# Kernel optimization log

Measured on AMD Instinct MI355X. Metric: run time of the kernel, lower is better.

## Reference

```python
import jax, jax.numpy as jnp
import numpy as np

N = 50000      # num_nodes
E = 12500      # num hyperedges
NNZ = 400000   # incidence pairs
OBS = 64
LAT = 64
STEPS = 20     # (t1 - t0) / dt = 1.0 / 0.05
DT = 0.05
SQRT_DT = DT ** 0.5
SIGMA_INIT = 0.1


def setup_inputs() -> dict:
    key = jax.random.key(0)
    ks = jax.random.split(key, 12)
    w = lambda k, o, i: jax.random.normal(k, (o, i), dtype=jnp.float32) * (1.0 / np.sqrt(i))
    return {
        "x": jax.random.normal(ks[0], (N, OBS), dtype=jnp.float32),
        "enc_w1": w(ks[1], LAT, OBS),
        "enc_b1": jnp.zeros((LAT,), jnp.float32),
        "enc_w2": w(ks[2], LAT, LAT),
        "enc_b2": jnp.zeros((LAT,), jnp.float32),
        "conv_w": w(ks[3], LAT, LAT),
        "conv_b": jnp.zeros((LAT,), jnp.float32),
        "sigma": SIGMA_INIT * jnp.ones((LAT,), jnp.float32),
        "dec_w1": w(ks[4], LAT, LAT),
        "dec_b1": jnp.zeros((LAT,), jnp.float32),
        "dec_w2": w(ks[5], OBS, LAT),
        "dec_b2": jnp.zeros((OBS,), jnp.float32),
        "node_idx": jax.random.randint(ks[6], (NNZ,), 0, N),
        "edge_idx": jax.random.randint(ks[7], (NNZ,), 0, E),
        "seed": 0,
    }


def _mlp(x, w1, b1, w2, b2):
    # eqx.nn.MLP depth=1: linear -> relu -> linear, applied per node (vmapped == matmul)
    return jax.nn.relu(x @ w1.T + b1) @ w2.T + b2


def reference(x, enc_w1, enc_b1, enc_w2, enc_b2, conv_w, conv_b, sigma,
              dec_w1, dec_b1, dec_w2, dec_b2, node_idx, edge_idx, seed):
    # incidence degree normalization (HGNN-style), computed once
    ones = jnp.ones((NNZ,), jnp.float32)
    edge_deg_inv = 1.0 / jnp.maximum(jax.ops.segment_sum(ones, edge_idx, num_segments=E), 1.0)
    node_deg_inv = 1.0 / jnp.maximum(jax.ops.segment_sum(ones, node_idx, num_segments=N), 1.0)

    def conv(y):
        m = y @ conv_w.T                                                    # [N, LAT]
        e = jax.ops.segment_sum(m[node_idx], edge_idx, num_segments=E)     # node -> hyperedge
        e = e * edge_deg_inv[:, None]
        out = jax.ops.segment_sum(e[edge_idx], node_idx, num_segments=N)   # hyperedge -> node
        return out * node_deg_inv[:, None] + conv_b

    def step(y, k):
        dw = jax.random.normal(k, (N, LAT), dtype=y.dtype)
        drift = jnp.tanh(conv(y))                       # activation(conv) drift
        y = y + drift * DT + sigma * SQRT_DT * dw       # Euler-Maruyama, diagonal noise
        return y, None

    z0 = _mlp(x, enc_w1, enc_b1, enc_w2, enc_b2)        # encode (n, obs) -> (n, lat)
    keys = jax.random.split(jax.random.key(seed), STEPS)
    z1, _ = jax.lax.scan(step, z0, keys)
    return _mlp(z1, dec_w1, dec_b1, dec_w2, dec_b2)     # decode at t1
```

## Files before the change

kernel.cpp:

```cpp
#include <hip/hip_runtime.h>
#include <stdint.h>

#define N_NODES 50000
#define N_EDGES 12500
#define NNZV    400000
#define STEPS   20
#define DT_F    0.05f
#define SQRTDT_F 0.22360679774997896f

__device__ __forceinline__ float rdlf(float v, int l) {
  return __uint_as_float(__builtin_amdgcn_readlane(__float_as_uint(v), (unsigned)l));
}
__device__ __forceinline__ int rfl(int v) {
  return (int)__builtin_amdgcn_readfirstlane((unsigned)v);
}

__device__ __forceinline__ void tf2x32(uint32_t k0, uint32_t k1,
                                       uint32_t x0, uint32_t x1,
                                       uint32_t& o0, uint32_t& o1) {
  uint32_t k2 = k0 ^ k1 ^ 0x1BD11BDAu;
#define TFR(r) { x0 += x1; x1 = (x1 << (r)) | (x1 >> (32 - (r))); x1 ^= x0; }
  x0 += k0; x1 += k1;
  TFR(13) TFR(15) TFR(26) TFR(6)   x0 += k1; x1 += k2 + 1u;
  TFR(17) TFR(29) TFR(16) TFR(24)  x0 += k2; x1 += k0 + 2u;
  TFR(13) TFR(15) TFR(26) TFR(6)   x0 += k0; x1 += k1 + 3u;
  TFR(17) TFR(29) TFR(16) TFR(24)  x0 += k1; x1 += k2 + 4u;
  TFR(13) TFR(15) TFR(26) TFR(6)   x0 += k2; x1 += k0 + 5u;
#undef TFR
  o0 = x0; o1 = x1;
}

__device__ __forceinline__ float erfinv_fast(float x) {
  float w = -__logf((1.0f - x) * (1.0f + x));
  float p;
  if (w < 5.0f) {
    w = w - 2.5f;
    p =              2.81022636e-08f;
    p = fmaf(p, w,   3.43273939e-07f);
    p = fmaf(p, w,  -3.5233877e-06f);
    p = fmaf(p, w,  -4.39150654e-06f);
    p = fmaf(p, w,   0.00021858087f);
    p = fmaf(p, w,  -0.00125372503f);
    p = fmaf(p, w,  -0.00417768164f);
    p = fmaf(p, w,   0.246640727f);
    p = fmaf(p, w,   1.50140941f);
  } else {
    w = sqrtf(w) - 3.0f;
    p =             -0.000200214257f;
    p = fmaf(p, w,   0.000100950558f);
    p = fmaf(p, w,   0.00134934322f);
    p = fmaf(p, w,  -0.00367342844f);
    p = fmaf(p, w,   0.00573950773f);
    p = fmaf(p, w,  -0.0076224613f);
    p = fmaf(p, w,   0.00943887047f);
    p = fmaf(p, w,   1.00167406f);
    p = fmaf(p, w,   2.83297682f);
  }
  return p * x;
}

__device__ __forceinline__ float bits_to_normal(uint32_t b) {
  float f = __uint_as_float((b >> 9) | 0x3f800000u) - 1.0f;
  const float lo = -0.99999994f;
  float u = fmaf(f, 2.0f, lo);
  u = fmaxf(u, lo);
  return 1.41421356237f * erfinv_fast(u);
}

__device__ __forceinline__ float fast_tanhf(float x) {
  float t = __expf(2.0f * x);
  return 1.0f - 2.0f / (t + 1.0f);
}

__global__ void k_keys(const int* __restrict__ seed, unsigned* __restrict__ keys) {
  int j = threadIdx.x;
  if (j < STEPS) {
    unsigned s = (unsigned)seed[0];
    unsigned o0, o1;
    tf2x32(0u, s, 0u, (unsigned)j, o0, o1);
    keys[2 * j] = o0; keys[2 * j + 1] = o1;
  }
}

__global__ void k_zero(int* __restrict__ p, int n) {
  int i = blockIdx.x * 256 + threadIdx.x;
  if (i < n) p[i] = 0;
}

__global__ void k_hist(const int* __restrict__ nidx, const int* __restrict__ eidx,
                       int* __restrict__ ecnt, int* __restrict__ ncnt) {
  int i = blockIdx.x * 256 + threadIdx.x;
  if (i < NNZV) {
    atomicAdd(&ecnt[eidx[i]], 1);
    atomicAdd(&ncnt[nidx[i]], 1);
  }
}

__global__ __launch_bounds__(256) void k_reduce(const int* __restrict__ cnt, int len,
                                                int* __restrict__ bsum) {
  __shared__ int sh[256];
  int b = blockIdx.x, tid = threadIdx.x;
  int base = b * 1024 + tid * 4;
  int s = 0;
#pragma unroll
  for (int j = 0; j < 4; ++j) {
    int i = base + j;
    if (i < len) s += cnt[i];
  }
  sh[tid] = s;
  __syncthreads();
  for (int off = 128; off > 0; off >>= 1) {
    if (tid < off) sh[tid] += sh[tid + off];
    __syncthreads();
  }
  if (tid == 0) bsum[b] = sh[0];
}

__global__ __launch_bounds__(256) void k_scanb(int* __restrict__ bsum, int nb) {
  __shared__ int sh[256];
  int tid = threadIdx.x;
  int v = (tid < nb) ? bsum[tid] : 0;
  sh[tid] = v;
  __syncthreads();
  for (int off = 1; off < 256; off <<= 1) {
    int t = (tid >= off) ? sh[tid - off] : 0;
    __syncthreads();
    sh[tid] += t;
    __syncthreads();
  }
  if (tid < nb) bsum[tid] = sh[tid] - v;
}

__global__ __launch_bounds__(256) void k_scatter(const int* __restrict__ cnt,
                                                 const int* __restrict__ bsum, int len,
                                                 int* __restrict__ start,
                                                 int* __restrict__ fill,
                                                 float* __restrict__ dinv) {
  __shared__ int sh[256];
  int b = blockIdx.x, tid = threadIdx.x;
  int base = b * 1024 + tid * 4;
  int c[4], lex[4];
  int s = 0;
#pragma unroll
  for (int j = 0; j < 4; ++j) {
    int i = base + j;
    c[j] = (i < len) ? cnt[i] : 0;
    lex[j] = s;
    s += c[j];
  }
  sh[tid] = s;
  __syncthreads();
  for (int off = 1; off < 256; off <<= 1) {
    int t = (tid >= off) ? sh[tid - off] : 0;
    __syncthreads();
    sh[tid] += t;
    __syncthreads();
  }
  int off0 = bsum[b] + sh[tid] - s;
#pragma unroll
  for (int j = 0; j < 4; ++j) {
    int i = base + j;
    if (i < len) {
      start[i] = off0 + lex[j];
      fill[i] = 0;
      dinv[i] = 1.0f / (float)(c[j] > 1 ? c[j] : 1);
    }
  }
}

__global__ void k_fill(const int* __restrict__ nidx, const int* __restrict__ eidx,
                       const int* __restrict__ estart, const int* __restrict__ nstart,
                       int* __restrict__ efill, int* __restrict__ nfill,
                       int* __restrict__ emem, int* __restrict__ nmem) {
  int i = blockIdx.x * 256 + threadIdx.x;
  if (i < NNZV) {
    int e = eidx[i], n = nidx[i];
    int pe = atomicAdd(&efill[e], 1);
    emem[estart[e] + pe] = n;
    int pn = atomicAdd(&nfill[n], 1);
    nmem[nstart[n] + pn] = e;
  }
}

__device__ __forceinline__ void stage_swz(const float* __restrict__ w,
                                          float* __restrict__ lds, int tid) {
  for (int idx = tid; idx < 4096; idx += 256) {
    int j = idx >> 6, k = idx & 63;
    lds[k * 64 + (j ^ k)] = w[idx];
  }
}

__device__ __forceinline__ void seg_gather_dual(const float* __restrict__ rows,
                                                const int* __restrict__ mem,
                                                int st0, int d0, int st1, int d1,
                                                int lane, float& out0, float& out1) {
  float a0 = 0.f, a1 = 0.f, b0 = 0.f, b1 = 0.f;
  int i0 = 0, i1 = 0;
  while (i0 + 8 <= d0 && i1 + 8 <= d1) {
    int A0 = mem[st0 + i0],     A1 = mem[st0 + i0 + 1];
    int A2 = mem[st0 + i0 + 2], A3 = mem[st0 + i0 + 3];
    int A4 = mem[st0 + i0 + 4], A5 = mem[st0 + i0 + 5];
    int A6 = mem[st0 + i0 + 6], A7 = mem[st0 + i0 + 7];
    int B0 = mem[st1 + i1],     B1 = mem[st1 + i1 + 1];
    int B2 = mem[st1 + i1 + 2], B3 = mem[st1 + i1 + 3];
    int B4 = mem[st1 + i1 + 4], B5 = mem[st1 + i1 + 5];
    int B6 = mem[st1 + i1 + 6], B7 = mem[st1 + i1 + 7];
    float x0 = rows[(size_t)A0 * 64 + lane], x1 = rows[(size_t)A1 * 64 + lane];
    float x2 = rows[(size_t)A2 * 64 + lane], x3 = rows[(size_t)A3 * 64 + lane];
    float x4 = rows[(size_t)A4 * 64 + lane], x5 = rows[(size_t)A5 * 64 + lane];
    float x6 = rows[(size_t)A6 * 64 + lane], x7 = rows[(size_t)A7 * 64 + lane];
    float z0 = rows[(size_t)B0 * 64 + lane], z1 = rows[(size_t)B1 * 64 + lane];
    float z2 = rows[(size_t)B2 * 64 + lane], z3 = rows[(size_t)B3 * 64 + lane];
    float z4 = rows[(size_t)B4 * 64 + lane], z5 = rows[(size_t)B5 * 64 + lane];
    float z6 = rows[(size_t)B6 * 64 + lane], z7 = rows[(size_t)B7 * 64 + lane];
    a0 += (x0 + x1) + (x2 + x3);
    a1 += (x4 + x5) + (x6 + x7);
    b0 += (z0 + z1) + (z2 + z3);
    b1 += (z4 + z5) + (z6 + z7);
    i0 += 8; i1 += 8;
  }
  for (; i0 + 8 <= d0; i0 += 8) {
    int A0 = mem[st0 + i0],     A1 = mem[st0 + i0 + 1];
    int A2 = mem[st0 + i0 + 2], A3 = mem[st0 + i0 + 3];
    int A4 = mem[st0 + i0 + 4], A5 = mem[st0 + i0 + 5];
    int A6 = mem[st0 + i0 + 6], A7 = mem[st0 + i0 + 7];
    float x0 = rows[(size_t)A0 * 64 + lane], x1 = rows[(size_t)A1 * 64 + lane];
    float x2 = rows[(size_t)A2 * 64 + lane], x3 = rows[(size_t)A3 * 64 + lane];
    float x4 = rows[(size_t)A4 * 64 + lane], x5 = rows[(size_t)A5 * 64 + lane];
    float x6 = rows[(size_t)A6 * 64 + lane], x7 = rows[(size_t)A7 * 64 + lane];
    a0 += (x0 + x1) + (x2 + x3);
    a1 += (x4 + x5) + (x6 + x7);
  }
  for (; i0 < d0; ++i0) a0 += rows[(size_t)mem[st0 + i0] * 64 + lane];
  for (; i1 + 8 <= d1; i1 += 8) {
    int B0 = mem[st1 + i1],     B1 = mem[st1 + i1 + 1];
    int B2 = mem[st1 + i1 + 2], B3 = mem[st1 + i1 + 3];
    int B4 = mem[st1 + i1 + 4], B5 = mem[st1 + i1 + 5];
    int B6 = mem[st1 + i1 + 6], B7 = mem[st1 + i1 + 7];
    float z0 = rows[(size_t)B0 * 64 + lane], z1 = rows[(size_t)B1 * 64 + lane];
    float z2 = rows[(size_t)B2 * 64 + lane], z3 = rows[(size_t)B3 * 64 + lane];
    float z4 = rows[(size_t)B4 * 64 + lane], z5 = rows[(size_t)B5 * 64 + lane];
    float z6 = rows[(size_t)B6 * 64 + lane], z7 = rows[(size_t)B7 * 64 + lane];
    b0 += (z0 + z1) + (z2 + z3);
    b1 += (z4 + z5) + (z6 + z7);
  }
  for (; i1 < d1; ++i1) b0 += rows[(size_t)mem[st1 + i1] * 64 + lane];
  out0 = a0 + a1;
  out1 = b0 + b1;
}

__global__ __launch_bounds__(256) void k_encoder(
    const float* __restrict__ x, const float* __restrict__ w1,
    const float* __restrict__ b1, const float* __restrict__ w2,
    const float* __restrict__ b2, float* __restrict__ y) {
  __shared__ float lw1[4096], lw2[4096];
  int tid = threadIdx.x;
  stage_swz(w1, lw1, tid);
  stage_swz(w2, lw2, tid);
  __syncthreads();
  int lane = tid & 63, wave = tid >> 6;
  float w1r[64], w2r[64];
#pragma unroll
  for (int k = 0; k < 64; ++k) {
    w1r[k] = lw1[k * 64 + (lane ^ k)];
    w2r[k] = lw2[k * 64 + (lane ^ k)];
  }
  float b1v = b1[lane], b2v = b2[lane];
  int gw = blockIdx.x * 4 + wave, nw = gridDim.x * 4;
  for (int n = gw; n < N_NODES; n += nw) {
    float xv = x[(size_t)n * 64 + lane];
    float a0 = 0.f, a1 = 0.f, a2 = 0.f, a3 = 0.f;
#pragma unroll
    for (int k = 0; k < 64; k += 4) {
      a0 = fmaf(rdlf(xv, k),     w1r[k],     a0);
      a1 = fmaf(rdlf(xv, k + 1), w1r[k + 1], a1);
      a2 = fmaf(rdlf(xv, k + 2), w1r[k + 2], a2);
      a3 = fmaf(rdlf(xv, k + 3), w1r[k + 3], a3);
    }
    float h = fmaxf((a0 + a1) + (a2 + a3) + b1v, 0.f);
    a0 = a1 = a2 = a3 = 0.f;
#pragma unroll
    for (int k = 0; k < 64; k += 4) {
      a0 = fmaf(rdlf(h, k),     w2r[k],     a0);
      a1 = fmaf(rdlf(h, k + 1), w2r[k + 1], a1);
      a2 = fmaf(rdlf(h, k + 2), w2r[k + 2], a2);
      a3 = fmaf(rdlf(h, k + 3), w2r[k + 3], a3);
    }
    y[(size_t)n * 64 + lane] = (a0 + a1) + (a2 + a3) + b2v;
  }
}

__global__ __launch_bounds__(256) void k_edge(
    const float* __restrict__ y, float* __restrict__ e,
    const int* __restrict__ estart, const int* __restrict__ ecnt,
    const int* __restrict__ emem, const float* __restrict__ edinv,
    const float* __restrict__ cw) {
  __shared__ float lcw[4096];
  int tid = threadIdx.x;
  stage_swz(cw, lcw, tid);
  __syncthreads();
  int lane = tid & 63, wave = tid >> 6;
  const int NE2 = N_EDGES / 2;
  int gw = blockIdx.x * 4 + wave, nw = gridDim.x * 4;
  for (int p = gw; p < NE2; p += nw) {
    int p0 = rfl(p);
    int e0 = p0, e1 = p0 + NE2;
    int st0 = estart[e0], d0 = ecnt[e0];
    int st1 = estart[e1], d1 = ecnt[e1];
    float div0 = edinv[e0], div1 = edinv[e1];
    float s0, s1;
    seg_gather_dual(y, emem, st0, d0, st1, d1, lane, s0, s1);
    float a00 = 0.f, a01 = 0.f, a10 = 0.f, a11 = 0.f;
#pragma unroll
    for (int k = 0; k < 64; k += 2) {
      float w0 = lcw[k * 64 + (lane ^ k)];
      float w1 = lcw[(k + 1) * 64 + (lane ^ (k + 1))];
      a00 = fmaf(rdlf(s0, k),     w0, a00);
      a10 = fmaf(rdlf(s1, k),     w0, a10);
      a01 = fmaf(rdlf(s0, k + 1), w1, a01);
      a11 = fmaf(rdlf(s1, k + 1), w1, a11);
    }
    e[(size_t)e0 * 64 + lane] = (a00 + a01) * div0;
    e[(size_t)e1 * 64 + lane] = (a10 + a11) * div1;
  }
}

__global__ __launch_bounds__(256) void k_node(
    const float* __restrict__ e, float* __restrict__ y,
    const int* __restrict__ nstart, const int* __restrict__ ncnt,
    const int* __restrict__ nmem, const float* __restrict__ ndinv,
    const float* __restrict__ cb, const float* __restrict__ sigma,
    const unsigned* __restrict__ keys, int s) {
  int tid = threadIdx.x;
  int lane = tid & 63, wave = tid >> 6;
  float cbv = cb[lane];
  float sgv = sigma[lane] * SQRTDT_F;
  unsigned ka = keys[2 * s], kb = keys[2 * s + 1];
  const int NP = N_NODES / 2;
  int gw = blockIdx.x * 4 + wave, nw = gridDim.x * 4;
  for (int p = gw; p < NP; p += nw) {
    int p0 = rfl(p);
    int n0 = p0, n1 = p0 + NP;
    int st0 = nstart[n0], d0 = ncnt[n0];
    int st1 = nstart[n1], d1 = ncnt[n1];
    float di0 = ndinv[n0], di1 = ndinv[n1];
    float y0 = y[(size_t)n0 * 64 + lane];
    float y1 = y[(size_t)n1 * 64 + lane];
    float s0, s1;
    seg_gather_dual(e, nmem, st0, d0, st1, d1, lane, s0, s1);
    uint32_t r0, r1, r2, r3;
    tf2x32(ka, kb, 0u, (unsigned)(n0 * 64 + lane), r0, r1);
    tf2x32(ka, kb, 0u, (unsigned)(n1 * 64 + lane), r2, r3);
    float dw0 = bits_to_normal(r0 ^ r1);
    float dw1 = bits_to_normal(r2 ^ r3);
    y0 = fmaf(fast_tanhf(fmaf(s0, di0, cbv)), DT_F, fmaf(sgv, dw0, y0));
    y1 = fmaf(fast_tanhf(fmaf(s1, di1, cbv)), DT_F, fmaf(sgv, dw1, y1));
    y[(size_t)n0 * 64 + lane] = y0;
    y[(size_t)n1 * 64 + lane] = y1;
  }
}

__global__ __launch_bounds__(256) void k_decoder(
    const float* __restrict__ y, const float* __restrict__ w1,
    const float* __restrict__ b1, const float* __restrict__ w2,
    const float* __restrict__ b2, float* __restrict__ out) {
  __shared__ float lw1[4096], lw2[4096];
  int tid = threadIdx.x;
  stage_swz(w1, lw1, tid);
  stage_swz(w2, lw2, tid);
  __syncthreads();
  int lane = tid & 63, wave = tid >> 6;
  float w1r[64], w2r[64];
#pragma unroll
  for (int k = 0; k < 64; ++k) {
    w1r[k] = lw1[k * 64 + (lane ^ k)];
    w2r[k] = lw2[k * 64 + (lane ^ k)];
  }
  float b1v = b1[lane], b2v = b2[lane];
  int gw = blockIdx.x * 4 + wave, nw = gridDim.x * 4;
  for (int n = gw; n < N_NODES; n += nw) {
    float xv = y[(size_t)n * 64 + lane];
    float a0 = 0.f, a1 = 0.f, a2 = 0.f, a3 = 0.f;
#pragma unroll
    for (int k = 0; k < 64; k += 4) {
      a0 = fmaf(rdlf(xv, k),     w1r[k],     a0);
      a1 = fmaf(rdlf(xv, k + 1), w1r[k + 1], a1);
      a2 = fmaf(rdlf(xv, k + 2), w1r[k + 2], a2);
      a3 = fmaf(rdlf(xv, k + 3), w1r[k + 3], a3);
    }
    float h = fmaxf((a0 + a1) + (a2 + a3) + b1v, 0.f);
    a0 = a1 = a2 = a3 = 0.f;
#pragma unroll
    for (int k = 0; k < 64; k += 4) {
      a0 = fmaf(rdlf(h, k),     w2r[k],     a0);
      a1 = fmaf(rdlf(h, k + 1), w2r[k + 1], a1);
      a2 = fmaf(rdlf(h, k + 2), w2r[k + 2], a2);
      a3 = fmaf(rdlf(h, k + 3), w2r[k + 3], a3);
    }
    out[(size_t)n * 64 + lane] = (a0 + a1) + (a2 + a3) + b2v;
  }
}

extern "C" void kernel_launch(void* const* d_in, const int* in_sizes, int n_in,
                              void* d_out, int out_size, void* d_ws, size_t ws_size,
                              hipStream_t stream) {
  (void)in_sizes; (void)n_in; (void)out_size; (void)ws_size;
  const float* x      = (const float*)d_in[0];
  const float* enc_w1 = (const float*)d_in[1];
  const float* enc_b1 = (const float*)d_in[2];
  const float* enc_w2 = (const float*)d_in[3];
  const float* enc_b2 = (const float*)d_in[4];
  const float* conv_w = (const float*)d_in[5];
  const float* conv_b = (const float*)d_in[6];
  const float* sigma  = (const float*)d_in[7];
  const float* dec_w1 = (const float*)d_in[8];
  const float* dec_b1 = (const float*)d_in[9];
  const float* dec_w2 = (const float*)d_in[10];
  const float* dec_b2 = (const float*)d_in[11];
  const int* node_idx = (const int*)d_in[12];
  const int* edge_idx = (const int*)d_in[13];
  const int* seed     = (const int*)d_in[14];

  char* wsb = (char*)d_ws;
  size_t off = 0;
  auto alloc = [&](size_t bytes) -> void* {
    void* p = wsb + off;
    off = (off + bytes + 255) & ~(size_t)255;
    return p;
  };
  float* y        = (float*)alloc((size_t)N_NODES * 64 * 4);
  float* e        = (float*)alloc((size_t)N_EDGES * 64 * 4);
  int* edge_cnt   = (int*)alloc((size_t)N_EDGES * 4);
  int* node_cnt   = (int*)alloc((size_t)N_NODES * 4);
  int* edge_start = (int*)alloc((size_t)N_EDGES * 4);
  int* node_start = (int*)alloc((size_t)N_NODES * 4);
  int* edge_fill  = (int*)alloc((size_t)N_EDGES * 4);
  int* node_fill  = (int*)alloc((size_t)N_NODES * 4);
  int* edge_mem   = (int*)alloc((size_t)NNZV * 4);
  int* node_mem   = (int*)alloc((size_t)NNZV * 4);
  float* edinv    = (float*)alloc((size_t)N_EDGES * 4);
  float* ndinv    = (float*)alloc((size_t)N_NODES * 4);
  unsigned* keys  = (unsigned*)alloc(2 * STEPS * 4);
  int* ebsum      = (int*)alloc(256 * 4);
  int* nbsum      = (int*)alloc(256 * 4);

  const int EB = (N_EDGES + 1023) / 1024;
  const int NB = (N_NODES + 1023) / 1024;

  dim3 b256(256);
  hipLaunchKernelGGL(k_keys, dim3(1), dim3(64), 0, stream, seed, keys);
  hipLaunchKernelGGL(k_zero, dim3((N_EDGES + 255) / 256), b256, 0, stream, edge_cnt, N_EDGES);
  hipLaunchKernelGGL(k_zero, dim3((N_NODES + 255) / 256), b256, 0, stream, node_cnt, N_NODES);
  hipLaunchKernelGGL(k_hist, dim3((NNZV + 255) / 256), b256, 0, stream,
                     node_idx, edge_idx, edge_cnt, node_cnt);
  hipLaunchKernelGGL(k_reduce, dim3(EB), b256, 0, stream, edge_cnt, N_EDGES, ebsum);
  hipLaunchKernelGGL(k_reduce, dim3(NB), b256, 0, stream, node_cnt, N_NODES, nbsum);
  hipLaunchKernelGGL(k_scanb, dim3(1), b256, 0, stream, ebsum, EB);
  hipLaunchKernelGGL(k_scanb, dim3(1), b256, 0, stream, nbsum, NB);
  hipLaunchKernelGGL(k_scatter, dim3(EB), b256, 0, stream,
                     edge_cnt, ebsum, N_EDGES, edge_start, edge_fill, edinv);
  hipLaunchKernelGGL(k_scatter, dim3(NB), b256, 0, stream,
                     node_cnt, nbsum, N_NODES, node_start, node_fill, ndinv);
  hipLaunchKernelGGL(k_fill, dim3((NNZV + 255) / 256), b256, 0, stream,
                     node_idx, edge_idx, edge_start, node_start,
                     edge_fill, node_fill, edge_mem, node_mem);
  hipLaunchKernelGGL(k_encoder, dim3(1024), b256, 0, stream,
                     x, enc_w1, enc_b1, enc_w2, enc_b2, y);
  for (int s = 0; s < STEPS; ++s) {
    hipLaunchKernelGGL(k_edge, dim3(1563), b256, 0, stream,
                       y, e, edge_start, edge_cnt, edge_mem, edinv, conv_w);
    hipLaunchKernelGGL(k_node, dim3(2048), b256, 0, stream,
                       e, y, node_start, node_cnt, node_mem, ndinv,
                       conv_b, sigma, keys, s);
  }
  hipLaunchKernelGGL(k_decoder, dim3(1024), b256, 0, stream,
                     y, dec_w1, dec_b1, dec_w2, dec_b2, (float*)d_out);
}
```

Baseline: 1.097 ms.

## Fuse SDE time-step loop into one persistent cooperative kernel with grid sync

Replaces the 40 separate edge/node kernel launches with one cooperative persistent kernel that loops over all steps, using grid-wide barriers between the edge-gather and node-update phases. Conv weights are staged into LDS once instead of every step. This removes per-launch overhead and the kernel-boundary drain between phases. In exchange, the grid is limited by occupancy, which may lower parallelism per phase, and adds grid.sync costs. The old launches remain as a fallback if the cooperative launch fails.

Measured after the change: 4.321 ms. +293.8%, slower.

```diff
diff --git a/kernel.cpp b/kernel.cpp
--- a/kernel.cpp
+++ b/kernel.cpp
@@ -1,5 +1,8 @@
 #include <hip/hip_runtime.h>
+#include <hip/hip_cooperative_groups.h>
 #include <stdint.h>
+
+namespace cg = cooperative_groups;
 
 #define N_NODES 50000
 #define N_EDGES 12500
@@ -290,18 +293,12 @@
   }
 }
 
-__global__ __launch_bounds__(256) void k_edge(
+__device__ __forceinline__ void edge_body(
     const float* __restrict__ y, float* __restrict__ e,
     const int* __restrict__ estart, const int* __restrict__ ecnt,
     const int* __restrict__ emem, const float* __restrict__ edinv,
-    const float* __restrict__ cw) {
-  __shared__ float lcw[4096];
-  int tid = threadIdx.x;
-  stage_swz(cw, lcw, tid);
-  __syncthreads();
-  int lane = tid & 63, wave = tid >> 6;
+    const float* __restrict__ lcw, int lane, int gw, int nw) {
   const int NE2 = N_EDGES / 2;
-  int gw = blockIdx.x * 4 + wave, nw = gridDim.x * 4;
   for (int p = gw; p < NE2; p += nw) {
     int p0 = rfl(p);
     int e0 = p0, e1 = p0 + NE2;
@@ -325,19 +322,12 @@
   }
 }
 
-__global__ __launch_bounds__(256) void k_node(
+__device__ __forceinline__ void node_body(
     const float* __restrict__ e, float* __restrict__ y,
     const int* __restrict__ nstart, const int* __restrict__ ncnt,
     const int* __restrict__ nmem, const float* __restrict__ ndinv,
-    const float* __restrict__ cb, const float* __restrict__ sigma,
-    const unsigned* __restrict__ keys, int s) {
-  int tid = threadIdx.x;
-  int lane = tid & 63, wave = tid >> 6;
-  float cbv = cb[lane];
-  float sgv = sigma[lane] * SQRTDT_F;
-  unsigned ka = keys[2 * s], kb = keys[2 * s + 1];
+    float cbv, float sgv, unsigned ka, unsigned kb, int lane, int gw, int nw) {
   const int NP = N_NODES / 2;
-  int gw = blockIdx.x * 4 + wave, nw = gridDim.x * 4;
   for (int p = gw; p < NP; p += nw) {
     int p0 = rfl(p);
     int n0 = p0, n1 = p0 + NP;
@@ -358,6 +348,61 @@
     y[(size_t)n0 * 64 + lane] = y0;
     y[(size_t)n1 * 64 + lane] = y1;
   }
+}
+
+__global__ __launch_bounds__(256) void k_step(
+    float* __restrict__ y, float* __restrict__ e,
+    const int* __restrict__ estart, const int* __restrict__ ecnt,
+    const int* __restrict__ emem, const float* __restrict__ edinv,
+    const int* __restrict__ nstart, const int* __restrict__ ncnt,
+    const int* __restrict__ nmem, const float* __restrict__ ndinv,
+    const float* __restrict__ cw, const float* __restrict__ cb,
+    const float* __restrict__ sigma, const unsigned* __restrict__ keys) {
+  cg::grid_group grid = cg::this_grid();
+  __shared__ float lcw[4096];
+  int tid = threadIdx.x;
+  stage_swz(cw, lcw, tid);
+  __syncthreads();
+  int lane = tid & 63, wave = tid >> 6;
+  float cbv = cb[lane];
+  float sgv = sigma[lane] * SQRTDT_F;
+  int gw = blockIdx.x * 4 + wave, nw = gridDim.x * 4;
+  for (int s = 0; s < STEPS; ++s) {
+    unsigned ka = keys[2 * s], kb = keys[2 * s + 1];
+    edge_body(y, e, estart, ecnt, emem, edinv, lcw, lane, gw, nw);
+    __threadfence();
+    grid.sync();
+    node_body(e, y, nstart, ncnt, nmem, ndinv, cbv, sgv, ka, kb, lane, gw, nw);
+    __threadfence();
+    grid.sync();
+  }
+}
+
+__global__ __launch_bounds__(256) void k_edge(
+    const float* __restrict__ y, float* __restrict__ e,
+    const int* __restrict__ estart, const int* __restrict__ ecnt,
+    const int* __restrict__ emem, const float* __restrict__ edinv,
+    const float* __restrict__ cw) {
+  __shared__ float lcw[4096];
+  int tid = threadIdx.x;
+  stage_swz(cw, lcw, tid);
+  __syncthreads();
+  int lane = tid & 63, wave = tid >> 6;
+  edge_body(y, e, estart, ecnt, emem, edinv, lcw, lane,
+            blockIdx.x * 4 + wave, gridDim.x * 4);
+}
+
+__global__ __launch_bounds__(256) void k_node(
+    const float* __restrict__ e, float* __restrict__ y,
+    const int* __restrict__ nstart, const int* __restrict__ ncnt,
+    const int* __restrict__ nmem, const float* __restrict__ ndinv,
+    const float* __restrict__ cb, const float* __restrict__ sigma,
+    const unsigned* __restrict__ keys, int s) {
+  int tid = threadIdx.x;
+  int lane = tid & 63, wave = tid >> 6;
+  node_body(e, y, nstart, ncnt, nmem, ndinv, cb[lane], sigma[lane] * SQRTDT_F,
+            keys[2 * s], keys[2 * s + 1], lane,
+            blockIdx.x * 4 + wave, gridDim.x * 4);
 }
 
 __global__ __launch_bounds__(256) void k_decoder(
@@ -466,12 +511,33 @@
                      edge_fill, node_fill, edge_mem, node_mem);
   hipLaunchKernelGGL(k_encoder, dim3(1024), b256, 0, stream,
                      x, enc_w1, enc_b1, enc_w2, enc_b2, y);
-  for (int s = 0; s < STEPS; ++s) {
-    hipLaunchKernelGGL(k_edge, dim3(1563), b256, 0, stream,
-                       y, e, edge_start, edge_cnt, edge_mem, edinv, conv_w);
-    hipLaunchKernelGGL(k_node, dim3(2048), b256, 0, stream,
-                       e, y, node_start, node_cnt, node_mem, ndinv,
-                       conv_b, sigma, keys, s);
+
+  int nb_per_cu = 0;
+  hipError_t occ_err = hipOccupancyMaxActiveBlocksPerMultiprocessor(
+      &nb_per_cu, (const void*)k_step, 256, 0);
+  bool coop_ok = false;
+  if (occ_err == hipSuccess && nb_per_cu >= 1) {
+    hipDeviceProp_t prop;
+    if (hipGetDeviceProperties(&prop, 0) == hipSuccess) {
+      int grid = nb_per_cu * prop.multiProcessorCount;
+      if (grid > 2048) grid = 2048;
+      void* args[] = { (void*)&y, (void*)&e, (void*)&edge_start, (void*)&edge_cnt,
+                       (void*)&edge_mem, (void*)&edinv, (void*)&node_start,
+                       (void*)&node_cnt, (void*)&node_mem, (void*)&ndinv,
+                       (void*)&conv_w, (void*)&conv_b, (void*)&sigma, (void*)&keys };
+      hipError_t lerr = hipLaunchCooperativeKernel(
+          (const void*)k_step, dim3(grid), dim3(256), args, 0, stream);
+      coop_ok = (lerr == hipSuccess);
+    }
+  }
+  if (!coop_ok) {
+    for (int s = 0; s < STEPS; ++s) {
+      hipLaunchKernelGGL(k_edge, dim3(1563), b256, 0, stream,
+                         y, e, edge_start, edge_cnt, edge_mem, edinv, conv_w);
+      hipLaunchKernelGGL(k_node, dim3(2048), b256, 0, stream,
+                         e, y, node_start, node_cnt, node_mem, ndinv,
+                         conv_b, sigma, keys, s);
+    }
   }
   hipLaunchKernelGGL(k_decoder, dim3(1024), b256, 0, stream,
                      y, dec_w1, dec_b1, dec_w2, dec_b2, (float*)d_out);
```
